# Optimization experiments

Hardware: AMD Instinct MI355X
Metric: run time of the kernel (lower is better)

The kernel has to match this reference:

```python
import jax, jax.numpy as jnp
import numpy as np

B, L, D_MODEL, N_HEADS = 2, 2048, 1024, 16
HEAD_DIM = D_MODEL // N_HEADS  # 64
PAD_START = (3 * L) // 4  # last quarter of keys are padding


def _rope_tables(seq_len, dim, base=10000.0, dtype=jnp.float32):
    inv_freq = 1.0 / (base ** (jnp.arange(0, dim, 2, dtype=jnp.float32) / dim))
    t = jnp.arange(seq_len, dtype=jnp.float32)
    freqs = jnp.einsum('i,j->ij', t, inv_freq)  # (L, dim/2)
    return jnp.cos(freqs).astype(dtype), jnp.sin(freqs).astype(dtype)


def _apply_rope(x, cos, sin):
    # x: (B, H, L, D); cos/sin: (L, D/2)
    cos = cos[None, None]
    sin = sin[None, None]
    x_even, x_odd = x[..., 0::2], x[..., 1::2]
    rot_even = x_even * cos - x_odd * sin
    rot_odd = x_even * sin + x_odd * cos
    return jnp.stack((rot_even, rot_odd), axis=-1).reshape(x.shape)


def setup_inputs() -> dict:
    key = jax.random.key(0)
    k_x, k_wqkv, k_bqkv, k_wout, k_bout = jax.random.split(key, 5)
    x = jax.random.normal(k_x, (B, L, D_MODEL), dtype=jnp.float32)
    Wqkv = jax.random.normal(k_wqkv, (3 * D_MODEL, D_MODEL), dtype=jnp.float32) * 0.02
    bqkv = jax.random.normal(k_bqkv, (3 * D_MODEL,), dtype=jnp.float32) * 0.02
    Wout = jax.random.normal(k_wout, (D_MODEL, D_MODEL), dtype=jnp.float32) * 0.02
    bout = jax.random.normal(k_bout, (D_MODEL,), dtype=jnp.float32) * 0.02
    # True = padded position (end of sequence padded)
    pad_mask = jnp.broadcast_to(jnp.arange(L) >= PAD_START, (B, L))
    return {"x": x, "pad_mask": pad_mask, "Wqkv": Wqkv, "bqkv": bqkv, "Wout": Wout, "bout": bout}


def reference(x, pad_mask, Wqkv, bqkv, Wout, bout):
    Bc, Lc, E = x.shape
    H, D = N_HEADS, HEAD_DIM
    qkv = x @ Wqkv.T + bqkv                       # (B, L, 3E)
    qkv = qkv.reshape(Bc, Lc, 3, H, D)
    q = jnp.transpose(qkv[:, :, 0], (0, 2, 1, 3))  # (B, H, L, D)
    k = jnp.transpose(qkv[:, :, 1], (0, 2, 1, 3))
    v = jnp.transpose(qkv[:, :, 2], (0, 2, 1, 3))
    cos, sin = _rope_tables(Lc, D, dtype=x.dtype)
    q = _apply_rope(q, cos, sin)
    k = _apply_rope(k, cos, sin)
    # Mask exactly as the torch module builds it: attn_mask = causal_upper | key_pad,
    # with torch bool-mask semantics (True = allowed to attend).
    causal_upper = jnp.triu(jnp.ones((Lc, Lc), dtype=bool), 1)[None, None]  # (1,1,L,L)
    key_pad = pad_mask[:, None, None, :]                                     # (B,1,1,L)
    allowed = causal_upper | key_pad                                         # (B,1,L,L)
    scale = 1.0 / jnp.sqrt(jnp.asarray(D, dtype=x.dtype))
    scores = jnp.einsum('bhqd,bhkd->bhqk', q, k) * scale
    scores = jnp.where(allowed, scores, -jnp.inf)
    attn = jax.nn.softmax(scores, axis=-1)
    out = jnp.einsum('bhqk,bhkd->bhqd', attn, v)   # (B, H, L, D)
    out = jnp.transpose(out, (0, 2, 1, 3)).reshape(Bc, Lc, E)
    return out @ Wout.T + bout
```

## Files before the change

### kernel.cpp

```cpp
#include <hip/hip_runtime.h>

#define BB 2
#define LL 2048
#define DM 1024
#define NH 16
#define HD 64
#define PAD_START 1536

typedef short bf16x8 __attribute__((ext_vector_type(8)));
typedef float f32x4 __attribute__((ext_vector_type(4)));

#define MFMA_B16(a, b, c) __builtin_amdgcn_mfma_f32_16x16x32_bf16(a, b, c, 0, 0, 0)

#define GLOAD_LDS16(g, l)                                            \
    __builtin_amdgcn_global_load_lds(                                \
        (const __attribute__((address_space(1))) void*)(g),          \
        (__attribute__((address_space(3))) void*)(l), 16, 0, 0)

__device__ __forceinline__ float bf2f(unsigned short u) {
    union { unsigned int i; float f; } v; v.i = ((unsigned int)u) << 16; return v.f;
}
__device__ __forceinline__ unsigned short f2bf(float f) {
    union { float f; unsigned int i; } v; v.f = f;
    unsigned int x = v.i;
    return (unsigned short)((x + 0x7fffu + ((x >> 16) & 1u)) >> 16);
}

__global__ __launch_bounds__(256) void split_kernel(
    const float* __restrict__ X, const float* __restrict__ Wq,
    const float* __restrict__ Wo,
    unsigned short* __restrict__ Xh,
    unsigned short* __restrict__ Wh,
    unsigned short* __restrict__ Woh,
    float* __restrict__ cosT, float* __restrict__ sinT)
{
    if (blockIdx.x >= 8192) {
        const int idx = (blockIdx.x - 8192) * 256 + threadIdx.x;
        const int l = idx >> 5, pp = idx & 31;
        const float LOG2_1E4 = 13.287712379549449f;
        const float invf = exp2f(-((float)pp) * (LOG2_1E4 / 32.0f));
        const float ang = (float)l * invf;
        float2 cs; cs.x = cosf(ang); cs.y = sinf(ang);
        ((float2*)cosT)[idx] = cs;
        return;
    }
    const size_t e = ((size_t)blockIdx.x * 256 + threadIdx.x) * 4;
    const float* src; unsigned short* dh; size_t o;
    if (e < 4194304)      { src = X;  dh = Xh;  o = e; }
    else if (e < 7340032) { src = Wq; dh = Wh;  o = e - 4194304; }
    else                  { src = Wo; dh = Woh; o = e - 7340032; }
    float4 v = *(const float4*)(src + o);
    ushort4 hv;
    hv.x = f2bf(v.x); hv.y = f2bf(v.y);
    hv.z = f2bf(v.z); hv.w = f2bf(v.w);
    *(ushort4*)(dh + o) = hv;
}

__device__ __forceinline__ void qk_frag(
    f32x4 cf, int r0, int bh, int d, float bv, float qscale,
    const float2* __restrict__ ct2,
    unsigned short* __restrict__ dst, bool odd)
{
    const int p = d >> 1;
#pragma unroll
    for (int e = 0; e < 4; ++e) {
        const int l = (r0 + e) & (LL - 1);
        const float x = cf[e] + bv;
        const float px = __shfl_xor(x, 1);
        const float2 cs = ct2[l * 32 + p];
        const float ve = odd ? px : x;
        const float vo = odd ? x : px;
        float res = odd ? (ve * cs.y + vo * cs.x) : (ve * cs.x - vo * cs.y);
        res *= qscale;
        const float other = __shfl_xor(res, 1);
        if (!odd) {
            const unsigned int pk = ((unsigned int)f2bf(res)) |
                                    (((unsigned int)f2bf(other)) << 16);
            *(unsigned int*)(dst + ((size_t)bh * LL + l) * HD + d) = pk;
        }
    }
}

__device__ __forceinline__ void v_frag(
    f32x4 cf, int l0, int bh, int d, float bv, unsigned short* __restrict__ vt)
{
    ushort4 pk;
    pk.x = f2bf(cf[0] + bv); pk.y = f2bf(cf[1] + bv);
    pk.z = f2bf(cf[2] + bv); pk.w = f2bf(cf[3] + bv);
    *(ushort4*)(vt + ((size_t)(bh * HD + d)) * LL + l0) = pk;
}

__device__ __forceinline__ void out_frag(
    f32x4 cf, int r0, int c, float bv, float* __restrict__ C)
{
#pragma unroll
    for (int e = 0; e < 4; ++e)
        C[(size_t)(r0 + e) * DM + c] = cf[e] + bv;
}

__global__ __launch_bounds__(512) void qkv_mfma(
    const unsigned short* __restrict__ Xh,
    const unsigned short* __restrict__ Wh,
    const float* __restrict__ bias,
    const float* __restrict__ cosT,
    unsigned short* __restrict__ qs, unsigned short* __restrict__ ks,
    unsigned short* __restrict__ vt)
{
    __shared__ unsigned short As[2 * 256 * 64];
    __shared__ unsigned short Bs[2 * 192 * 64];

    const int bid = blockIdx.y * 16 + blockIdx.x;
    const int xcd = bid & 7;
    const int i   = bid >> 3;
    const int mt  = (xcd & 3) * 4 + (i & 3);
    const int nt  = (xcd >> 2) * 8 + (i >> 2);
    const int m0 = mt * 256, n0 = nt * 192;

    const int t = threadIdx.x;
    const int lane = t & 63;
    const int w = t >> 6;
    const int wm = w >> 2;
    const int wn = w & 3;
    const int lm = lane & 15;
    const int quad = lane >> 4;

    const int rop = lane >> 3;
    const int sw  = ((lane & 7) ^ rop) * 8;
    const unsigned short* ga = Xh + (size_t)(m0 + w * 32 + rop) * 1024 + sw;
    const unsigned short* gb = Wh + (size_t)(n0 + w * 24 + rop) * 1024 + sw;
    unsigned short* lA = As + (w * 32) * 64;
    unsigned short* lB = Bs + (w * 24) * 64;

    const int o1 = (quad ^ (lm & 7)) * 8;
    const int o2 = ((quad + 4) ^ (lm & 7)) * 8;
    const int ar = (wm * 128 + lm) * 64;
    const int br = (wn * 48 + lm) * 64;

    f32x4 acc[8][3];
#pragma unroll
    for (int mf = 0; mf < 8; ++mf)
#pragma unroll
        for (int nf = 0; nf < 3; ++nf) acc[mf][nf] = (f32x4){0.f,0.f,0.f,0.f};

#define STG(ABO, BBO, k0)                                                 \
    do {                                                                  \
        GLOAD_LDS16(ga + (k0),             lA + (ABO));                   \
        GLOAD_LDS16(ga + (k0) +  8 * 1024, lA + (ABO) +  8 * 64);         \
        GLOAD_LDS16(ga + (k0) + 16 * 1024, lA + (ABO) + 16 * 64);         \
        GLOAD_LDS16(ga + (k0) + 24 * 1024, lA + (ABO) + 24 * 64);         \
        GLOAD_LDS16(gb + (k0),             lB + (BBO));                   \
        GLOAD_LDS16(gb + (k0) +  8 * 1024, lB + (BBO) +  8 * 64);         \
        GLOAD_LDS16(gb + (k0) + 16 * 1024, lB + (BBO) + 16 * 64);         \
    } while (0)

#define TILE(ABO, BBO, SG, KS, VMN)                                      \
    {                                                                     \
        bf16x8 af[8][2]; bf16x8 bfr[3][2];                                \
        _Pragma("unroll")                                                 \
        for (int mf = 0; mf < 8; ++mf) {                                  \
            af[mf][0] = *(const bf16x8*)(As + (ABO) + ar + mf * 1024 + o1);\
            af[mf][1] = *(const bf16x8*)(As + (ABO) + ar + mf * 1024 + o2);\
        }                                                                 \
        _Pragma("unroll")                                                 \
        for (int nf = 0; nf < 3; ++nf) {                                  \
            bfr[nf][0] = *(const bf16x8*)(Bs + (BBO) + br + nf * 1024 + o1);\
            bfr[nf][1] = *(const bf16x8*)(Bs + (BBO) + br + nf * 1024 + o2);\
        }                                                                 \
        asm volatile("s_waitcnt lgkmcnt(0)" ::: "memory");                \
        __builtin_amdgcn_sched_barrier(0);                                \
        __builtin_amdgcn_s_barrier();                                     \
        if (SG) { STG(ABO, BBO, KS); }      \
        asm volatile("s_waitcnt vmcnt(" VMN ")" ::: "memory");            \
        __builtin_amdgcn_sched_barrier(0);                                \
        __builtin_amdgcn_s_barrier();                                     \
        __builtin_amdgcn_s_setprio(1);                                    \
        _Pragma("unroll")                                                 \
        for (int mf = 0; mf < 8; ++mf) {                                  \
            _Pragma("unroll")                                             \
            for (int nf = 0; nf < 3; ++nf) {                              \
                acc[mf][nf] = MFMA_B16(af[mf][0], bfr[nf][0], acc[mf][nf]);\
                acc[mf][nf] = MFMA_B16(af[mf][1], bfr[nf][1], acc[mf][nf]);\
            }                                                             \
        }                                                                 \
        __builtin_amdgcn_s_setprio(0);                                    \
    }

    STG(0, 0, 0);
    STG(16384, 12288, 64);
    asm volatile("s_waitcnt vmcnt(7)" ::: "memory");
    __builtin_amdgcn_sched_barrier(0);
    __builtin_amdgcn_s_barrier();

    for (int k0 = 0; k0 < 896; k0 += 128) {
        TILE(0,     0,     1, k0 + 128, "7")
        TILE(16384, 12288, 1, k0 + 192, "7")
    }
    TILE(0,     0,     0, 0, "0")
    TILE(16384, 12288, 0, 0, "0")
#undef TILE
#undef STG

    const int bi = m0 >> 11;
    const int rbase = m0 + wm * 128;
    const int cbase = n0 + wn * 48;
    const bool odd = (lm & 1) != 0;
    const float2* ct2 = (const float2*)cosT;

#pragma unroll
    for (int nf = 0; nf < 3; ++nf) {
        const int col0 = cbase + nf * 16;
        const int s = col0 >> 10;
        const int h = (col0 & 1023) >> 6;
        const int bh = bi * NH + h;
        const int d = (col0 & 63) + lm;
        const float bv = bias[col0 + lm];
        if (s == 2) {
#pragma unroll
            for (int mf = 0; mf < 8; ++mf)
                v_frag(acc[mf][nf], (rbase + mf * 16 + quad * 4) & (LL - 1),
                       bh, d, bv, vt);
        } else {
            unsigned short* dst = (s == 0) ? qs : ks;
            const float qscale = (s == 0) ? 0.125f : 1.0f;
#pragma unroll
            for (int mf = 0; mf < 8; ++mf)
                qk_frag(acc[mf][nf], rbase + mf * 16 + quad * 4, bh,
                        d, bv, qscale, ct2, dst, odd);
        }
    }
}

__global__ __launch_bounds__(256) void attn_mfma(
    const unsigned short* __restrict__ qs,
    const unsigned short* __restrict__ ks,
    const unsigned short* __restrict__ vt,
    unsigned short* __restrict__ aoh)
{
    __shared__ unsigned short Ks[2][64 * 64];
    __shared__ unsigned short Vs[2][64 * 64];
    __shared__ unsigned short Pl[4][16 * 72];

    const int bid = blockIdx.y * 32 + blockIdx.x;
    const int xcd = bid & 7;
    const int j   = bid >> 3;
    const int bh  = xcd * 4 + (j & 3);
    const int qt  = ((j >> 2) + bh) & 31;
    const int q0 = qt * 64;
    const int b = bh >> 4, h = bh & (NH - 1);
    const int tid = threadIdx.x;
    const int w = tid >> 6;
    const int lane = tid & 63;
    const int lm = lane & 15;
    const int quad = lane >> 4;
    const int qw0 = q0 + w * 16;

    const unsigned short* qbase = qs + ((size_t)bh * LL + qw0 + lm) * HD + quad * 8;
    const bf16x8 qf0 = *(const bf16x8*)(qbase);
    const bf16x8 qf1 = *(const bf16x8*)(qbase + 32);

    f32x4 O[4];
#pragma unroll
    for (int dd = 0; dd < 4; ++dd) O[dd] = (f32x4){0.f, 0.f, 0.f, 0.f};
    float lrow[4] = {0.f, 0.f, 0.f, 0.f};

    const unsigned short* kbase = ks + (size_t)bh * LL * HD;
    const unsigned short* vtb   = vt + (size_t)bh * HD * LL;
    unsigned short* pw = &Pl[w][0];

    const int rop = lane >> 3;
    const int sw8 = ((lane & 7) ^ rop) * 8;
    const int r0 = w * 16 + rop;
    const int r1 = w * 16 + 8 + rop;
    const int o1 = (quad ^ (lm & 7)) * 8;
    const int o2 = ((quad + 4) ^ (lm & 7)) * 8;

#define ASTAGE(BUF, KK)                                                      \
    do {                                                                     \
        GLOAD_LDS16(kbase + (size_t)((KK) + r0) * HD + sw8,                  \
                    &Ks[BUF][0] + (w * 2) * 512);                            \
        GLOAD_LDS16(kbase + (size_t)((KK) + r1) * HD + sw8,                  \
                    &Ks[BUF][0] + (w * 2 + 1) * 512);                        \
        GLOAD_LDS16(vtb + (size_t)r0 * LL + (KK) + sw8,                      \
                    &Vs[BUF][0] + (w * 2) * 512);                            \
        GLOAD_LDS16(vtb + (size_t)r1 * LL + (KK) + sw8,                      \
                    &Vs[BUF][0] + (w * 2 + 1) * 512);                        \
    } while (0)

    const int t0 = ((q0 < PAD_START) ? q0 : PAD_START) >> 6;

    ASTAGE(t0 & 1, t0 * 64);
    __syncthreads();

    for (int tt = t0; tt < 32; ++tt) {
        const int k0 = tt * 64;
        const int cur = tt & 1;
        const unsigned short* Kc = &Ks[cur][0];
        const unsigned short* Vc = &Vs[cur][0];

        {
            const int kn = ((tt + 1) < 32 ? (tt + 1) : 31) * 64;
            ASTAGE(cur ^ 1, kn);
        }

        f32x4 sfrag[4];
#pragma unroll
        for (int c = 0; c < 4; ++c) {
            const bf16x8 kf0 = *(const bf16x8*)(Kc + (c * 16 + lm) * 64 + o1);
            const bf16x8 kf1 = *(const bf16x8*)(Kc + (c * 16 + lm) * 64 + o2);
            f32x4 z = (f32x4){0.f, 0.f, 0.f, 0.f};
            z = MFMA_B16(qf0, kf0, z);
            z = MFMA_B16(qf1, kf1, z);
            sfrag[c] = z;
        }
        if (tt == t0 && q0 < PAD_START) {
#pragma unroll
            for (int c = 0; c < 4; ++c) {
                const int kg = k0 + c * 16 + lm;
#pragma unroll
                for (int r = 0; r < 4; ++r) {
                    const int qg = qw0 + quad * 4 + r;
                    if (kg <= qg) sfrag[c][r] = -1e30f;
                }
            }
        }
#pragma unroll
        for (int r = 0; r < 4; ++r) {
#pragma unroll
            for (int c = 0; c < 4; ++c) {
                const float p = __expf(sfrag[c][r]);
                lrow[r] += p;
                pw[(quad * 4 + r) * 72 + c * 16 + lm] = f2bf(p);
            }
        }
        const bf16x8 a0 = *(const bf16x8*)(pw + lm * 72 + quad * 8);
        const bf16x8 a1 = *(const bf16x8*)(pw + lm * 72 + 32 + quad * 8);
#pragma unroll
        for (int dd = 0; dd < 4; ++dd) {
            const bf16x8 b0 = *(const bf16x8*)(Vc + (dd * 16 + lm) * 64 + o1);
            const bf16x8 b1 = *(const bf16x8*)(Vc + (dd * 16 + lm) * 64 + o2);
            O[dd] = MFMA_B16(a0, b0, O[dd]);
            O[dd] = MFMA_B16(a1, b1, O[dd]);
        }

        __syncthreads();
    }
#undef ASTAGE

#pragma unroll
    for (int r = 0; r < 4; ++r) {
        float rs = lrow[r];
        rs += __shfl_xor(rs, 1);
        rs += __shfl_xor(rs, 2);
        rs += __shfl_xor(rs, 4);
        rs += __shfl_xor(rs, 8);
        lrow[r] = rs;
    }

#pragma unroll
    for (int r = 0; r < 4; ++r) {
        const float inv = 1.0f / lrow[r];
        const int qg = qw0 + quad * 4 + r;
        const size_t base = ((size_t)(b * LL + qg)) * DM + h * HD;
#pragma unroll
        for (int dd = 0; dd < 4; ++dd)
            aoh[base + dd * 16 + lm] = f2bf(O[dd][r] * inv);
    }
}

__global__ __launch_bounds__(256) void out_mfma(
    const unsigned short* __restrict__ Ah,
    const unsigned short* __restrict__ Wh,
    const float* __restrict__ bias, float* __restrict__ C)
{
    __shared__ unsigned short As[128 * 64];
    __shared__ unsigned short Bs[128 * 64];
    const int n0 = blockIdx.x * 128;
    const int m0 = blockIdx.y * 128;

    f32x4 c00 = {0,0,0,0}, c01 = {0,0,0,0}, c02 = {0,0,0,0}, c03 = {0,0,0,0};
    f32x4 c10 = {0,0,0,0}, c11 = {0,0,0,0}, c12 = {0,0,0,0}, c13 = {0,0,0,0};
    f32x4 c20 = {0,0,0,0}, c21 = {0,0,0,0}, c22 = {0,0,0,0}, c23 = {0,0,0,0};
    f32x4 c30 = {0,0,0,0}, c31 = {0,0,0,0}, c32 = {0,0,0,0}, c33 = {0,0,0,0};

    const int t = threadIdx.x;
    const int lane = t & 63;
    const int w = t >> 6;
    const int wm = (w >> 1) << 6;
    const int wn = (w & 1) << 6;
    const int lm = lane & 15;
    const int quad = lane >> 4;

    const int rop = lane >> 3;
    const int sw  = ((lane & 7) ^ rop) * 8;
    const unsigned short* ga = Ah + (size_t)(m0 + w * 32 + rop) * 1024 + sw;
    const unsigned short* gb = Wh + (size_t)(n0 + w * 32 + rop) * 1024 + sw;
    unsigned short* lA = As + (w * 32) * 64;
    unsigned short* lB = Bs + (w * 32) * 64;

    const int o1 = (quad ^ (lm & 7)) * 8;
    const int o2 = ((quad + 4) ^ (lm & 7)) * 8;
    const int arow = (wm + lm) * 64;
    const int brow = (wn + lm) * 64;

    for (int k0 = 0; k0 < 1024; k0 += 64) {
        __syncthreads();
        GLOAD_LDS16(ga + k0,             lA);
        GLOAD_LDS16(ga + k0 +  8 * 1024, lA +  8 * 64);
        GLOAD_LDS16(ga + k0 + 16 * 1024, lA + 16 * 64);
        GLOAD_LDS16(ga + k0 + 24 * 1024, lA + 24 * 64);
        GLOAD_LDS16(gb + k0,             lB);
        GLOAD_LDS16(gb + k0 +  8 * 1024, lB +  8 * 64);
        GLOAD_LDS16(gb + k0 + 16 * 1024, lB + 16 * 64);
        GLOAD_LDS16(gb + k0 + 24 * 1024, lB + 24 * 64);
        __syncthreads();
        {
            bf16x8 a0 = *(const bf16x8*)(As + arow +  0 * 64 + o1);
            bf16x8 a1 = *(const bf16x8*)(As + arow + 16 * 64 + o1);
            bf16x8 a2 = *(const bf16x8*)(As + arow + 32 * 64 + o1);
            bf16x8 a3 = *(const bf16x8*)(As + arow + 48 * 64 + o1);
            bf16x8 b0 = *(const bf16x8*)(Bs + brow +  0 * 64 + o1);
            bf16x8 b1 = *(const bf16x8*)(Bs + brow + 16 * 64 + o1);
            bf16x8 b2 = *(const bf16x8*)(Bs + brow + 32 * 64 + o1);
            bf16x8 b3 = *(const bf16x8*)(Bs + brow + 48 * 64 + o1);
            c00 = MFMA_B16(a0, b0, c00); c01 = MFMA_B16(a0, b1, c01);
            c02 = MFMA_B16(a0, b2, c02); c03 = MFMA_B16(a0, b3, c03);
            c10 = MFMA_B16(a1, b0, c10); c11 = MFMA_B16(a1, b1, c11);
            c12 = MFMA_B16(a1, b2, c12); c13 = MFMA_B16(a1, b3, c13);
            c20 = MFMA_B16(a2, b0, c20); c21 = MFMA_B16(a2, b1, c21);
            c22 = MFMA_B16(a2, b2, c22); c23 = MFMA_B16(a2, b3, c23);
            c30 = MFMA_B16(a3, b0, c30); c31 = MFMA_B16(a3, b1, c31);
            c32 = MFMA_B16(a3, b2, c32); c33 = MFMA_B16(a3, b3, c33);
        }
        {
            bf16x8 a0 = *(const bf16x8*)(As + arow +  0 * 64 + o2);
            bf16x8 a1 = *(const bf16x8*)(As + arow + 16 * 64 + o2);
            bf16x8 a2 = *(const bf16x8*)(As + arow + 32 * 64 + o2);
            bf16x8 a3 = *(const bf16x8*)(As + arow + 48 * 64 + o2);
            bf16x8 b0 = *(const bf16x8*)(Bs + brow +  0 * 64 + o2);
            bf16x8 b1 = *(const bf16x8*)(Bs + brow + 16 * 64 + o2);
            bf16x8 b2 = *(const bf16x8*)(Bs + brow + 32 * 64 + o2);
            bf16x8 b3 = *(const bf16x8*)(Bs + brow + 48 * 64 + o2);
            c00 = MFMA_B16(a0, b0, c00); c01 = MFMA_B16(a0, b1, c01);
            c02 = MFMA_B16(a0, b2, c02); c03 = MFMA_B16(a0, b3, c03);
            c10 = MFMA_B16(a1, b0, c10); c11 = MFMA_B16(a1, b1, c11);
            c12 = MFMA_B16(a1, b2, c12); c13 = MFMA_B16(a1, b3, c13);
            c20 = MFMA_B16(a2, b0, c20); c21 = MFMA_B16(a2, b1, c21);
            c22 = MFMA_B16(a2, b2, c22); c23 = MFMA_B16(a2, b3, c23);
            c30 = MFMA_B16(a3, b0, c30); c31 = MFMA_B16(a3, b1, c31);
            c32 = MFMA_B16(a3, b2, c32); c33 = MFMA_B16(a3, b3, c33);
        }
    }

#define CSTORE(rt, ct) \
    out_frag(c##rt##ct, m0 + wm + rt * 16 + quad * 4, \
             n0 + wn + ct * 16 + lm, bias[n0 + wn + ct * 16 + lm], C);
    CSTORE(0,0) CSTORE(0,1) CSTORE(0,2) CSTORE(0,3)
    CSTORE(1,0) CSTORE(1,1) CSTORE(1,2) CSTORE(1,3)
    CSTORE(2,0) CSTORE(2,1) CSTORE(2,2) CSTORE(2,3)
    CSTORE(3,0) CSTORE(3,1) CSTORE(3,2) CSTORE(3,3)
#undef CSTORE
}

extern "C" void kernel_launch(void* const* d_in, const int* in_sizes, int n_in,
                              void* d_out, int out_size, void* d_ws, size_t ws_size,
                              hipStream_t stream)
{
    const float* x    = (const float*)d_in[0];
    const float* Wqkv = (const float*)d_in[2];
    const float* bqkv = (const float*)d_in[3];
    const float* Wout = (const float*)d_in[4];
    const float* bout = (const float*)d_in[5];
    float* out = (float*)d_out;

    unsigned short* p = (unsigned short*)d_ws;
    const size_t SZ = (size_t)BB * NH * LL * HD;
    unsigned short* qsb = p; p += SZ;
    unsigned short* ksb = p; p += SZ;
    unsigned short* vtb = p; p += SZ;
    unsigned short* Xhi = p; p += SZ;
    unsigned short* Whi = p; p += (size_t)3145728;
    unsigned short* Wohi = p; p += (size_t)1048576;
    float* cosT = (float*)p; p += (size_t)4 * 65536;

    split_kernel<<<8448, 256, 0, stream>>>(x, Wqkv, Wout,
                                           Xhi, Whi, Wohi, cosT, nullptr);
    dim3 g1(16, 16);
    qkv_mfma<<<g1, 512, 0, stream>>>(Xhi, Whi, bqkv, cosT,
                                     qsb, ksb, vtb);
    dim3 g2(32, 32);
    attn_mfma<<<g2, 256, 0, stream>>>(qsb, ksb, vtb, Xhi);
    dim3 g3(8, 32);
    out_mfma<<<g3, 256, 0, stream>>>(Xhi, Wohi, bout, out);
}
```

Baseline: 216.5 us.

## Load K/V fragments directly from global memory instead of staging through LDS

Removes the double-buffered LDS staging of K and V tiles and the per-iteration block barrier. Each wave now loads its MFMA operand fragments for K and V straight from global memory into registers. This cuts LDS traffic and synchronization, but each of the four waves fetches the same K/V data separately. It also loses the overlap that the prefetch gave, so latency now depends on L1/L2 hits.

Result: slower. 298.8 us (+38.0%).

```diff
diff --git a/kernel.cpp b/kernel.cpp
--- a/kernel.cpp
+++ b/kernel.cpp
@@ -236,8 +236,6 @@
     const unsigned short* __restrict__ vt,
     unsigned short* __restrict__ aoh)
 {
-    __shared__ unsigned short Ks[2][64 * 64];
-    __shared__ unsigned short Vs[2][64 * 64];
     __shared__ unsigned short Pl[4][16 * 72];
 
     const int bid = blockIdx.y * 32 + blockIdx.x;
@@ -267,49 +265,35 @@
     const unsigned short* vtb   = vt + (size_t)bh * HD * LL;
     unsigned short* pw = &Pl[w][0];
 
-    const int rop = lane >> 3;
-    const int sw8 = ((lane & 7) ^ rop) * 8;
-    const int r0 = w * 16 + rop;
-    const int r1 = w * 16 + 8 + rop;
-    const int o1 = (quad ^ (lm & 7)) * 8;
-    const int o2 = ((quad + 4) ^ (lm & 7)) * 8;
-
-#define ASTAGE(BUF, KK)                                                      \
-    do {                                                                     \
-        GLOAD_LDS16(kbase + (size_t)((KK) + r0) * HD + sw8,                  \
-                    &Ks[BUF][0] + (w * 2) * 512);                            \
-        GLOAD_LDS16(kbase + (size_t)((KK) + r1) * HD + sw8,                  \
-                    &Ks[BUF][0] + (w * 2 + 1) * 512);                        \
-        GLOAD_LDS16(vtb + (size_t)r0 * LL + (KK) + sw8,                      \
-                    &Vs[BUF][0] + (w * 2) * 512);                            \
-        GLOAD_LDS16(vtb + (size_t)r1 * LL + (KK) + sw8,                      \
-                    &Vs[BUF][0] + (w * 2 + 1) * 512);                        \
-    } while (0)
+    const unsigned short* kp0 = kbase + (size_t)lm * HD + quad * 8;
+    const unsigned short* vp0 = vtb + (size_t)lm * LL + quad * 8;
 
     const int t0 = ((q0 < PAD_START) ? q0 : PAD_START) >> 6;
-
-    ASTAGE(t0 & 1, t0 * 64);
-    __syncthreads();
 
     for (int tt = t0; tt < 32; ++tt) {
         const int k0 = tt * 64;
-        const int cur = tt & 1;
-        const unsigned short* Kc = &Ks[cur][0];
-        const unsigned short* Vc = &Vs[cur][0];
-
-        {
-            const int kn = ((tt + 1) < 32 ? (tt + 1) : 31) * 64;
-            ASTAGE(cur ^ 1, kn);
+
+        bf16x8 kf[4][2];
+#pragma unroll
+        for (int c = 0; c < 4; ++c) {
+            const unsigned short* kp = kp0 + (size_t)(k0 + c * 16) * HD;
+            kf[c][0] = *(const bf16x8*)(kp);
+            kf[c][1] = *(const bf16x8*)(kp + 32);
+        }
+        bf16x8 vf[4][2];
+#pragma unroll
+        for (int dd = 0; dd < 4; ++dd) {
+            const unsigned short* vp = vp0 + (size_t)(dd * 16) * LL + k0;
+            vf[dd][0] = *(const bf16x8*)(vp);
+            vf[dd][1] = *(const bf16x8*)(vp + 32);
         }
 
         f32x4 sfrag[4];
 #pragma unroll
         for (int c = 0; c < 4; ++c) {
-            const bf16x8 kf0 = *(const bf16x8*)(Kc + (c * 16 + lm) * 64 + o1);
-            const bf16x8 kf1 = *(const bf16x8*)(Kc + (c * 16 + lm) * 64 + o2);
             f32x4 z = (f32x4){0.f, 0.f, 0.f, 0.f};
-            z = MFMA_B16(qf0, kf0, z);
-            z = MFMA_B16(qf1, kf1, z);
+            z = MFMA_B16(qf0, kf[c][0], z);
+            z = MFMA_B16(qf1, kf[c][1], z);
             sfrag[c] = z;
         }
         if (tt == t0 && q0 < PAD_START) {
@@ -336,15 +320,10 @@
         const bf16x8 a1 = *(const bf16x8*)(pw + lm * 72 + 32 + quad * 8);
 #pragma unroll
         for (int dd = 0; dd < 4; ++dd) {
-            const bf16x8 b0 = *(const bf16x8*)(Vc + (dd * 16 + lm) * 64 + o1);
-            const bf16x8 b1 = *(const bf16x8*)(Vc + (dd * 16 + lm) * 64 + o2);
-            O[dd] = MFMA_B16(a0, b0, O[dd]);
-            O[dd] = MFMA_B16(a1, b1, O[dd]);
-        }
-
-        __syncthreads();
-    }
-#undef ASTAGE
+            O[dd] = MFMA_B16(a0, vf[dd][0], O[dd]);
+            O[dd] = MFMA_B16(a1, vf[dd][1], O[dd]);
+        }
+    }
 
 #pragma unroll
     for (int r = 0; r < 4; ++r) {
```

## Pair complementary query tiles per attention block to balance triangular work

Applied to the files above, without the earlier changes.

Each attention block now processes two query tiles, qp and 31-qp, which share the same streamed K/V tiles, halving the grid. Under the inverted causal mask the key range runs from the query tile to the end, so pairing short and long tiles evens out per-block work and reuses each K/V load for both tiles. In exchange it roughly doubles accumulator registers and P scratch in LDS, which may lower occupancy, and it leaves only 512 blocks.

Result: faster. 200.1 us (-7.6%).

```diff
diff --git a/kernel.cpp b/kernel.cpp
--- a/kernel.cpp
+++ b/kernel.cpp
@@ -238,34 +238,45 @@
 {
     __shared__ unsigned short Ks[2][64 * 64];
     __shared__ unsigned short Vs[2][64 * 64];
-    __shared__ unsigned short Pl[4][16 * 72];
-
-    const int bid = blockIdx.y * 32 + blockIdx.x;
+    __shared__ unsigned short Pl[8][16 * 72];
+
+    const int bid = blockIdx.y * 16 + blockIdx.x;
     const int xcd = bid & 7;
     const int j   = bid >> 3;
     const int bh  = xcd * 4 + (j & 3);
-    const int qt  = ((j >> 2) + bh) & 31;
-    const int q0 = qt * 64;
+    const int qp  = j >> 2;
+    const int qtA = qp;
+    const int qtB = 31 - qp;
+    const int q0A = qtA * 64, q0B = qtB * 64;
     const int b = bh >> 4, h = bh & (NH - 1);
     const int tid = threadIdx.x;
     const int w = tid >> 6;
     const int lane = tid & 63;
     const int lm = lane & 15;
     const int quad = lane >> 4;
-    const int qw0 = q0 + w * 16;
-
-    const unsigned short* qbase = qs + ((size_t)bh * LL + qw0 + lm) * HD + quad * 8;
-    const bf16x8 qf0 = *(const bf16x8*)(qbase);
-    const bf16x8 qf1 = *(const bf16x8*)(qbase + 32);
-
-    f32x4 O[4];
-#pragma unroll
-    for (int dd = 0; dd < 4; ++dd) O[dd] = (f32x4){0.f, 0.f, 0.f, 0.f};
-    float lrow[4] = {0.f, 0.f, 0.f, 0.f};
+    const int qwA = q0A + w * 16;
+    const int qwB = q0B + w * 16;
+
+    const unsigned short* qbA = qs + ((size_t)bh * LL + qwA + lm) * HD + quad * 8;
+    const unsigned short* qbB = qs + ((size_t)bh * LL + qwB + lm) * HD + quad * 8;
+    const bf16x8 qfA0 = *(const bf16x8*)(qbA);
+    const bf16x8 qfA1 = *(const bf16x8*)(qbA + 32);
+    const bf16x8 qfB0 = *(const bf16x8*)(qbB);
+    const bf16x8 qfB1 = *(const bf16x8*)(qbB + 32);
+
+    f32x4 OA[4], OB[4];
+#pragma unroll
+    for (int dd = 0; dd < 4; ++dd) {
+        OA[dd] = (f32x4){0.f, 0.f, 0.f, 0.f};
+        OB[dd] = (f32x4){0.f, 0.f, 0.f, 0.f};
+    }
+    float lrA[4] = {0.f, 0.f, 0.f, 0.f};
+    float lrB[4] = {0.f, 0.f, 0.f, 0.f};
 
     const unsigned short* kbase = ks + (size_t)bh * LL * HD;
     const unsigned short* vtb   = vt + (size_t)bh * HD * LL;
-    unsigned short* pw = &Pl[w][0];
+    unsigned short* pwA = &Pl[w][0];
+    unsigned short* pwB = &Pl[w + 4][0];
 
     const int rop = lane >> 3;
     const int sw8 = ((lane & 7) ^ rop) * 8;
@@ -286,60 +297,101 @@
                     &Vs[BUF][0] + (w * 2 + 1) * 512);                        \
     } while (0)
 
-    const int t0 = ((q0 < PAD_START) ? q0 : PAD_START) >> 6;
-
-    ASTAGE(t0 & 1, t0 * 64);
+    const int t0A = qtA;
+    const int t0B = (qtB < 24) ? qtB : 24;
+
+    ASTAGE(t0A & 1, t0A * 64);
     __syncthreads();
 
-    for (int tt = t0; tt < 32; ++tt) {
+    for (int tt = t0A; tt < 32; ++tt) {
         const int k0 = tt * 64;
         const int cur = tt & 1;
         const unsigned short* Kc = &Ks[cur][0];
         const unsigned short* Vc = &Vs[cur][0];
+        const bool doB = (tt >= t0B);
 
         {
             const int kn = ((tt + 1) < 32 ? (tt + 1) : 31) * 64;
             ASTAGE(cur ^ 1, kn);
         }
 
-        f32x4 sfrag[4];
+        f32x4 sfA[4], sfB[4];
 #pragma unroll
         for (int c = 0; c < 4; ++c) {
             const bf16x8 kf0 = *(const bf16x8*)(Kc + (c * 16 + lm) * 64 + o1);
             const bf16x8 kf1 = *(const bf16x8*)(Kc + (c * 16 + lm) * 64 + o2);
-            f32x4 z = (f32x4){0.f, 0.f, 0.f, 0.f};
-            z = MFMA_B16(qf0, kf0, z);
-            z = MFMA_B16(qf1, kf1, z);
-            sfrag[c] = z;
-        }
-        if (tt == t0 && q0 < PAD_START) {
+            f32x4 zA = (f32x4){0.f, 0.f, 0.f, 0.f};
+            zA = MFMA_B16(qfA0, kf0, zA);
+            zA = MFMA_B16(qfA1, kf1, zA);
+            sfA[c] = zA;
+            f32x4 zB = (f32x4){0.f, 0.f, 0.f, 0.f};
+            if (doB) {
+                zB = MFMA_B16(qfB0, kf0, zB);
+                zB = MFMA_B16(qfB1, kf1, zB);
+            }
+            sfB[c] = zB;
+        }
+        if (tt == t0A) {
 #pragma unroll
             for (int c = 0; c < 4; ++c) {
                 const int kg = k0 + c * 16 + lm;
 #pragma unroll
                 for (int r = 0; r < 4; ++r) {
-                    const int qg = qw0 + quad * 4 + r;
-                    if (kg <= qg) sfrag[c][r] = -1e30f;
+                    if (kg <= qwA + quad * 4 + r) sfA[c][r] = -1e30f;
                 }
             }
         }
+        if (doB && tt == t0B && qtB < 24) {
+#pragma unroll
+            for (int c = 0; c < 4; ++c) {
+                const int kg = k0 + c * 16 + lm;
+#pragma unroll
+                for (int r = 0; r < 4; ++r) {
+                    if (kg <= qwB + quad * 4 + r) sfB[c][r] = -1e30f;
+                }
+            }
+        }
+
 #pragma unroll
         for (int r = 0; r < 4; ++r) {
 #pragma unroll
             for (int c = 0; c < 4; ++c) {
-                const float p = __expf(sfrag[c][r]);
-                lrow[r] += p;
-                pw[(quad * 4 + r) * 72 + c * 16 + lm] = f2bf(p);
+                const float pA = __expf(sfA[c][r]);
+                lrA[r] += pA;
+                pwA[(quad * 4 + r) * 72 + c * 16 + lm] = f2bf(pA);
             }
         }
-        const bf16x8 a0 = *(const bf16x8*)(pw + lm * 72 + quad * 8);
-        const bf16x8 a1 = *(const bf16x8*)(pw + lm * 72 + 32 + quad * 8);
+        if (doB) {
+#pragma unroll
+            for (int r = 0; r < 4; ++r) {
+#pragma unroll
+                for (int c = 0; c < 4; ++c) {
+                    const float pB = __expf(sfB[c][r]);
+                    lrB[r] += pB;
+                    pwB[(quad * 4 + r) * 72 + c * 16 + lm] = f2bf(pB);
+                }
+            }
+        }
+
+        const bf16x8 aA0 = *(const bf16x8*)(pwA + lm * 72 + quad * 8);
+        const bf16x8 aA1 = *(const bf16x8*)(pwA + lm * 72 + 32 + quad * 8);
 #pragma unroll
         for (int dd = 0; dd < 4; ++dd) {
             const bf16x8 b0 = *(const bf16x8*)(Vc + (dd * 16 + lm) * 64 + o1);
             const bf16x8 b1 = *(const bf16x8*)(Vc + (dd * 16 + lm) * 64 + o2);
-            O[dd] = MFMA_B16(a0, b0, O[dd]);
-            O[dd] = MFMA_B16(a1, b1, O[dd]);
+            OA[dd] = MFMA_B16(aA0, b0, OA[dd]);
+            OA[dd] = MFMA_B16(aA1, b1, OA[dd]);
+        }
+        if (doB) {
+            const bf16x8 aB0 = *(const bf16x8*)(pwB + lm * 72 + quad * 8);
+            const bf16x8 aB1 = *(const bf16x8*)(pwB + lm * 72 + 32 + quad * 8);
+#pragma unroll
+            for (int dd = 0; dd < 4; ++dd) {
+                const bf16x8 b0 = *(const bf16x8*)(Vc + (dd * 16 + lm) * 64 + o1);
+                const bf16x8 b1 = *(const bf16x8*)(Vc + (dd * 16 + lm) * 64 + o2);
+                OB[dd] = MFMA_B16(aB0, b0, OB[dd]);
+                OB[dd] = MFMA_B16(aB1, b1, OB[dd]);
+            }
         }
 
         __syncthreads();
@@ -348,22 +400,34 @@
 
 #pragma unroll
     for (int r = 0; r < 4; ++r) {
-        float rs = lrow[r];
-        rs += __shfl_xor(rs, 1);
-        rs += __shfl_xor(rs, 2);
-        rs += __shfl_xor(rs, 4);
-        rs += __shfl_xor(rs, 8);
-        lrow[r] = rs;
+        float rsA = lrA[r];
+        rsA += __shfl_xor(rsA, 1);
+        rsA += __shfl_xor(rsA, 2);
+        rsA += __shfl_xor(rsA, 4);
+        rsA += __shfl_xor(rsA, 8);
+        lrA[r] = rsA;
+        float rsB = lrB[r];
+        rsB += __shfl_xor(rsB, 1);
+        rsB += __shfl_xor(rsB, 2);
+        rsB += __shfl_xor(rsB, 4);
+        rsB += __shfl_xor(rsB, 8);
+        lrB[r] = rsB;
     }
 
 #pragma unroll
     for (int r = 0; r < 4; ++r) {
-        const float inv = 1.0f / lrow[r];
-        const int qg = qw0 + quad * 4 + r;
-        const size_t base = ((size_t)(b * LL + qg)) * DM + h * HD;
+        const float invA = 1.0f / lrA[r];
+        const int qgA = qwA + quad * 4 + r;
+        const size_t baseA = ((size_t)(b * LL + qgA)) * DM + h * HD;
 #pragma unroll
         for (int dd = 0; dd < 4; ++dd)
-            aoh[base + dd * 16 + lm] = f2bf(O[dd][r] * inv);
+            aoh[baseA + dd * 16 + lm] = f2bf(OA[dd][r] * invA);
+        const float invB = 1.0f / lrB[r];
+        const int qgB = qwB + quad * 4 + r;
+        const size_t baseB = ((size_t)(b * LL + qgB)) * DM + h * HD;
+#pragma unroll
+        for (int dd = 0; dd < 4; ++dd)
+            aoh[baseB + dd * 16 + lm] = f2bf(OB[dd][r] * invB);
     }
 }
 
@@ -487,7 +551,7 @@
     dim3 g1(16, 16);
     qkv_mfma<<<g1, 512, 0, stream>>>(Xhi, Whi, bqkv, cosT,
                                      qsb, ksb, vtb);
-    dim3 g2(32, 32);
+    dim3 g2(16, 32);
     attn_mfma<<<g2, 256, 0, stream>>>(qsb, ksb, vtb, Xhi);
     dim3 g3(8, 32);
     out_mfma<<<g3, 256, 0, stream>>>(Xhi, Wohi, bout, out);
```
